# Optimization experiments

Hardware: AMD Instinct MI355X
Metric: run time of the kernel (lower is better)

Reference implementation:

```python
import jax, jax.numpy as jnp
import numpy as np
from jax.scipy.special import logsumexp

N = 8192       # number of vectors being quantized
E_DIM = 768    # embedding dim
N_E = 1024     # codebook size per layer
SK_EPS = (0.0, 0.003, 0.003, 0.003)
SK_ITERS = 100
BETA = 1.0


def setup_inputs() -> dict:
    key = jax.random.key(0)
    ks = jax.random.split(key, 5)
    inp = {"x": jax.random.normal(ks[0], (N, E_DIM), jnp.float32)}
    for i in range(4):
        inp[f"codebook_{i}"] = jax.random.normal(ks[i + 1], (N_E, E_DIM), jnp.float32) * 0.02
    return inp


def _sq_dist(x, e):
    # squared euclidean cdist: [N, K]
    return (jnp.sum(x * x, axis=1, keepdims=True)
            + jnp.sum(e * e, axis=1)[None, :]
            - 2.0 * (x @ e.T))


def _sinkhorn_indices(d, eps, iters):
    # log-domain Sinkhorn on Q = exp(-d/eps); constants (1/K, 1/B) dropped
    # since they do not affect the final argmax assignment.
    logQ = -d / eps  # [N, K]

    def body(_, lq):
        lq = lq - logsumexp(lq, axis=0, keepdims=True)  # normalize per code over batch
        lq = lq - logsumexp(lq, axis=1, keepdims=True)  # normalize per sample over codes
        return lq

    logQ = jax.lax.fori_loop(0, iters, body, logQ)
    return jnp.argmax(logQ, axis=1)


def _vq_layer(residual, codebook, eps):
    d = _sq_dist(residual, codebook)
    if eps > 0:
        indices = _sinkhorn_indices(d, eps, SK_ITERS)
    else:
        indices = jnp.argmin(d, axis=1)
    x_q = codebook[indices]  # gather [N, E_DIM]
    sg = jax.lax.stop_gradient
    loss = jnp.mean((sg(x_q) - residual) ** 2) + BETA * jnp.mean((x_q - sg(residual)) ** 2)
    x_q = residual + sg(x_q - residual)  # straight-through estimator
    return x_q, loss, indices


def reference(x, codebook_0, codebook_1, codebook_2, codebook_3):
    codebooks = (codebook_0, codebook_1, codebook_2, codebook_3)
    residual = x
    x_q = jnp.zeros_like(x)
    losses, all_idx = [], []
    for cb, eps in zip(codebooks, SK_EPS):
        xr, loss, idx = _vq_layer(residual, cb, eps)
        residual = residual - xr
        x_q = x_q + xr
        losses.append(loss)
        all_idx.append(idx)
    mean_loss = jnp.stack(losses).mean()
    indices = jnp.stack(all_idx, axis=-1)  # [N, num_quantizers]
    return x_q, mean_loss, indices
```

## Files before the change

### kernel.cpp

```cpp
#include <hip/hip_runtime.h>
#include <math.h>

#define N_VEC   8192
#define EDIM    768
#define NCODES  1024
#define SKITERS 100
#define ROWS_PB 32
#define CHUNKS  (N_VEC / ROWS_PB)
#define DYN_LDS ((32 * NCODES + 32) * 4)

__device__ __forceinline__ void ast(float* p, float v) {
  __hip_atomic_store(p, v, __ATOMIC_RELAXED, __HIP_MEMORY_SCOPE_AGENT);
}
__device__ __forceinline__ float ald(float* p) {
  return __hip_atomic_load(p, __ATOMIC_RELAXED, __HIP_MEMORY_SCOPE_AGENT);
}
__device__ __forceinline__ void asti(int* p, int v) {
  __hip_atomic_store(p, v, __ATOMIC_RELAXED, __HIP_MEMORY_SCOPE_AGENT);
}
__device__ __forceinline__ int aldi(int* p) {
  return __hip_atomic_load(p, __ATOMIC_RELAXED, __HIP_MEMORY_SCOPE_AGENT);
}
union MS { unsigned long long u; float2 f; };
__device__ __forceinline__ void astms(unsigned long long* p, float m, float s) {
  MS x; x.f.x = m; x.f.y = s;
  __hip_atomic_store(p, x.u, __ATOMIC_RELAXED, __HIP_MEMORY_SCOPE_AGENT);
}
__device__ __forceinline__ float2 aldms(unsigned long long* p) {
  MS x; x.u = __hip_atomic_load(p, __ATOMIC_RELAXED, __HIP_MEMORY_SCOPE_AGENT);
  return x.f;
}

__device__ __forceinline__ float np_base96_sq(const float* a) {
  float r[8];
#pragma unroll
  for (int j = 0; j < 8; ++j) r[j] = __fmul_rn(a[j], a[j]);
  for (int i = 8; i < 96; i += 8) {
#pragma unroll
    for (int j = 0; j < 8; ++j) r[j] = __fadd_rn(r[j], __fmul_rn(a[i + j], a[i + j]));
  }
  float c01 = __fadd_rn(r[0], r[1]);
  float c23 = __fadd_rn(r[2], r[3]);
  float c45 = __fadd_rn(r[4], r[5]);
  float c67 = __fadd_rn(r[6], r[7]);
  return __fadd_rn(__fadd_rn(c01, c23), __fadd_rn(c45, c67));
}
__device__ __forceinline__ float np_ssq768(const float* a) {
  float L[8];
#pragma unroll
  for (int t = 0; t < 8; ++t) L[t] = np_base96_sq(a + 96 * t);
  float a01 = __fadd_rn(L[0], L[1]);
  float a23 = __fadd_rn(L[2], L[3]);
  float a45 = __fadd_rn(L[4], L[5]);
  float a67 = __fadd_rn(L[6], L[7]);
  return __fadd_rn(__fadd_rn(a01, a23), __fadd_rn(a45, a67));
}

__global__ __launch_bounds__(64) void rows_ssq(const float* __restrict__ a,
                                               float* __restrict__ out, int nrows) {
  int row = blockIdx.x * 64 + threadIdx.x;
  if (row < nrows) out[row] = np_ssq768(a + (size_t)row * EDIM);
}

#define BM 128
#define BN 128
#define BK 16
template <bool LAYER0>
__global__ __launch_bounds__(256) void gemm_d(const float* __restrict__ A,
                                              const float* __restrict__ B,
                                              const float* __restrict__ sumrr,
                                              const float* __restrict__ sumee,
                                              float* __restrict__ V) {
  __shared__ float As[BK][BM];
  __shared__ float Bs[BK][BN];
  int tid = threadIdx.x;
  int bm = blockIdx.y * BM;
  int bn = blockIdx.x * BN;
  int lr = tid >> 1;
  int lc = (tid & 1) << 3;
  const float* Ap = A + (size_t)(bm + lr) * EDIM + lc;
  const float* Bp = B + (size_t)(bn + lr) * EDIM + lc;
  float acc[8][8];
#pragma unroll
  for (int i = 0; i < 8; ++i)
#pragma unroll
    for (int j = 0; j < 8; ++j) acc[i][j] = 0.f;
  int ty = tid >> 4, tx = tid & 15;
  for (int k0 = 0; k0 < EDIM; k0 += BK) {
    float4 a0 = *(const float4*)(Ap + k0);
    float4 a1 = *(const float4*)(Ap + k0 + 4);
    float4 b0 = *(const float4*)(Bp + k0);
    float4 b1 = *(const float4*)(Bp + k0 + 4);
    __syncthreads();
    As[lc + 0][lr] = a0.x; As[lc + 1][lr] = a0.y; As[lc + 2][lr] = a0.z; As[lc + 3][lr] = a0.w;
    As[lc + 4][lr] = a1.x; As[lc + 5][lr] = a1.y; As[lc + 6][lr] = a1.z; As[lc + 7][lr] = a1.w;
    Bs[lc + 0][lr] = b0.x; Bs[lc + 1][lr] = b0.y; Bs[lc + 2][lr] = b0.z; Bs[lc + 3][lr] = b0.w;
    Bs[lc + 4][lr] = b1.x; Bs[lc + 5][lr] = b1.y; Bs[lc + 6][lr] = b1.z; Bs[lc + 7][lr] = b1.w;
    __syncthreads();
#pragma unroll
    for (int k = 0; k < BK; ++k) {
      float av[8], bv[8];
      *(float4*)(av)     = *(const float4*)(&As[k][ty * 8]);
      *(float4*)(av + 4) = *(const float4*)(&As[k][ty * 8 + 4]);
      *(float4*)(bv)     = *(const float4*)(&Bs[k][tx * 8]);
      *(float4*)(bv + 4) = *(const float4*)(&Bs[k][tx * 8 + 4]);
#pragma unroll
      for (int i = 0; i < 8; ++i)
#pragma unroll
        for (int j = 0; j < 8; ++j) acc[i][j] = __fmaf_rn(av[i], bv[j], acc[i][j]);
    }
  }
#pragma unroll
  for (int i = 0; i < 8; ++i) {
    int row = bm + ty * 8 + i;
    float srr = sumrr[row];
    float* Vp = V + (size_t)row * NCODES + bn + tx * 8;
#pragma unroll
    for (int j = 0; j < 8; ++j) {
      int col = bn + tx * 8 + j;
      float s1 = __fadd_rn(srr, sumee[col]);
      float dv = __fsub_rn(s1, __fmul_rn(2.0f, acc[i][j]));
      Vp[j] = LAYER0 ? dv : __fdiv_rn(-dv, 0.003f);
    }
  }
}

__device__ __forceinline__ void accf(float w, float& m, float& s) {
  float d = __fsub_rn(w, m);
  float e = expf(-fabsf(d));
  bool gt = (w > m);
  s = gt ? __fadd_rn(__fmul_rn(s, e), 1.0f) : __fadd_rn(s, e);
  m = gt ? w : m;
}
__device__ __forceinline__ void mergef(float mo, float so, float& m, float& s) {
  float mn = fmaxf(m, mo);
  if (mn == -INFINITY) { s = 0.f; return; }
  float d = __fsub_rn(mo, m);
  float e = expf(-fabsf(d));
  bool gt = (mo > m);
  s = gt ? __fadd_rn(__fmul_rn(s, e), so) : __fadd_rn(s, __fmul_rn(so, e));
  m = mn;
}

__global__ __launch_bounds__(1024) void sk_persist(float* __restrict__ lq,
                                                   unsigned long long* __restrict__ part,
                                                   float* __restrict__ colL,
                                                   int* __restrict__ parr,
                                                   int* __restrict__ cready,
                                                   int* __restrict__ xarr,
                                                   int* __restrict__ xdone) {
  extern __shared__ float lds[];
  float (*vL)[NCODES] = (float(*)[NCODES])lds;
  float* rowLs = lds + 32 * NCODES;
  int tid = threadIdx.x, b = blockIdx.x;
  int wave = tid >> 6, lane = tid & 63;
  int r0 = b * ROWS_PB;

  float v[32];
#pragma unroll
  for (int r = 0; r < 32; ++r) v[r] = lq[(size_t)(r0 + r) * NCODES + tid];

#define COLCHAIN_ARRIVE(GEN)                                                  \
  do {                                                                        \
    float m = -INFINITY, s = 0.f;                                             \
    _Pragma("unroll")                                                         \
    for (int r = 0; r < 32; ++r) accf(v[r], m, s);                            \
    astms(&part[(size_t)b * NCODES + tid], m, s);                             \
    asm volatile("s_waitcnt vmcnt(0)" ::: "memory");                          \
    __syncthreads();                                                          \
    if (tid == 0) asti(&parr[b * 16], (GEN));                                 \
  } while (0)

  COLCHAIN_ARRIVE(1);

  for (int t = 0; t < SKITERS; ++t) {
    int gen = t + 1;

    if (wave == 0) {
      if (b < 8) {
        if (lane < 32) {
          int* fl = &parr[(b * 32 + lane) * 16];
          while (aldi(fl) < gen) __builtin_amdgcn_s_sleep(1);
        }
        asm volatile("" ::: "memory");
        if (lane == 0) asti(&xarr[b * 16], gen);
      }
      if (lane < 8) {
        int* fl = &xarr[lane * 16];
        while (aldi(fl) < gen) __builtin_amdgcn_s_sleep(1);
      }
      asm volatile("" ::: "memory");
      float m = -INFINITY, s = 0.f;
      if (lane < 32) {
        int colj = lane >> 3, grp = lane & 7;
        int col = 4 * b + colj;
#pragma unroll
        for (int qb = 0; qb < 32; qb += 16) {
          float2 pv[16];
#pragma unroll
          for (int q = 0; q < 16; ++q)
            pv[q] = aldms(&part[(size_t)(grp * 32 + qb + q) * NCODES + col]);
#pragma unroll
          for (int q = 0; q < 16; ++q) mergef(pv[q].x, pv[q].y, m, s);
        }
      }
      float mm = -INFINITY, ss = 0.f;
#pragma unroll
      for (int g2 = 0; g2 < 8; ++g2) {
        float mo = __shfl(m, ((lane & 3) << 3) + g2, 64);
        float so = __shfl(s, ((lane & 3) << 3) + g2, 64);
        mergef(mo, so, mm, ss);
      }
      if (lane < 4) ast(&colL[4 * b + lane], __fadd_rn(logf(ss), mm));
      asm volatile("s_waitcnt vmcnt(0)" ::: "memory");
      if (lane == 0) asti(&cready[b * 16], gen);
      if (b < 8) {
        if (lane < 32) {
          int* fl = &cready[(b * 32 + lane) * 16];
          while (aldi(fl) < gen) __builtin_amdgcn_s_sleep(1);
        }
        asm volatile("" ::: "memory");
        if (lane == 0) asti(&xdone[b * 16], gen);
      }
      if (lane < 8) {
        int* fl = &xdone[lane * 16];
        while (aldi(fl) < gen) __builtin_amdgcn_s_sleep(1);
      }
      asm volatile("" ::: "memory");
    }
    __syncthreads();

    float cl = ald(&colL[tid]);
#pragma unroll
    for (int r = 0; r < 32; ++r) {
      v[r] = __fsub_rn(v[r], cl);
      vL[r][tid] = v[r];
    }
    __syncthreads();

#pragma unroll
    for (int rr = 0; rr < 2; ++rr) {
      int row = wave * 2 + rr;
      float vals[16];
#pragma unroll
      for (int k = 0; k < 16; ++k) vals[k] = vL[row][lane + (k << 6)];
      float mx = vals[0];
#pragma unroll
      for (int k = 1; k < 16; ++k) mx = fmaxf(mx, vals[k]);
      for (int off = 32; off; off >>= 1) mx = fmaxf(mx, __shfl_xor(mx, off, 64));
      float s = 0.f;
#pragma unroll
      for (int k = 0; k < 16; ++k) s = __fadd_rn(s, expf(__fsub_rn(vals[k], mx)));
      for (int off = 32; off; off >>= 1) s = __fadd_rn(s, __shfl_xor(s, off, 64));
      if (lane == 0) rowLs[row] = __fadd_rn(logf(s), mx);
    }
    __syncthreads();
#pragma unroll
    for (int r = 0; r < 32; ++r) v[r] = __fsub_rn(v[r], rowLs[r]);

    if (t < SKITERS - 1) COLCHAIN_ARRIVE(gen + 1);
  }

#pragma unroll
  for (int r = 0; r < 32; ++r) lq[(size_t)(r0 + r) * NCODES + tid] = v[r];
#undef COLCHAIN_ARRIVE
}

template <int MODE>
__global__ __launch_bounds__(256) void epi(const float* __restrict__ V,
                                           const float* __restrict__ rin,
                                           const float* __restrict__ cb,
                                           float* __restrict__ rout,
                                           double* __restrict__ rowssq,
                                           float* __restrict__ idx_out,
                                           int layer) {
  int i = blockIdx.x;
  int tid = threadIdx.x;
  const float* Vrow = V + (size_t)i * NCODES;
  float bv = MODE ? -INFINITY : INFINITY;
  int bj = 0;
  for (int j = tid; j < NCODES; j += 256) {
    float v = Vrow[j];
    bool better = MODE ? (v > bv) : (v < bv);
    if (better) { bv = v; bj = j; }
  }
  __shared__ float sv[256];
  __shared__ int   sj[256];
  sv[tid] = bv; sj[tid] = bj;
  __syncthreads();
  for (int st = 128; st; st >>= 1) {
    if (tid < st) {
      float v2 = sv[tid + st]; int j2 = sj[tid + st];
      bool better = MODE ? (v2 > sv[tid]) : (v2 < sv[tid]);
      if (better || (v2 == sv[tid] && j2 < sj[tid])) { sv[tid] = v2; sj[tid] = j2; }
    }
    __syncthreads();
  }
  int idx = sj[0];
  const float* crow = cb + (size_t)idx * EDIM;
  double p = 0.0;
  for (int c = tid; c < EDIM; c += 256) {
    float rn = __fsub_rn(rin[(size_t)i * EDIM + c], crow[c]);
    rout[(size_t)i * EDIM + c] = rn;
    p += (double)rn * (double)rn;
  }
  for (int off = 32; off; off >>= 1) p += __shfl_xor(p, off, 64);
  __shared__ double wsum[4];
  if ((tid & 63) == 0) wsum[tid >> 6] = p;
  __syncthreads();
  if (tid == 0) {
    rowssq[i] = wsum[0] + wsum[1] + wsum[2] + wsum[3];
    idx_out[(size_t)i * 4 + layer] = (float)idx;
  }
}

__global__ __launch_bounds__(1024) void loss_final(const double* __restrict__ rowssq,
                                                   float* __restrict__ out_loss) {
  int tid = threadIdx.x;
  __shared__ double acc[16];
  __shared__ double ltot;
  if (tid == 0) ltot = 0.0;
  __syncthreads();
  for (int l = 0; l < 4; ++l) {
    double p = 0.0;
    for (int i = tid; i < N_VEC; i += 1024) p += rowssq[l * N_VEC + i];
    for (int off = 32; off; off >>= 1) p += __shfl_xor(p, off, 64);
    if ((tid & 63) == 0) acc[tid >> 6] = p;
    __syncthreads();
    if (tid == 0) {
      double sl = 0.0;
      for (int w = 0; w < 16; ++w) sl += acc[w];
      ltot += 2.0 * sl / ((double)N_VEC * (double)EDIM);
    }
    __syncthreads();
  }
  if (tid == 0) out_loss[0] = (float)(ltot * 0.25);
}

__global__ __launch_bounds__(256) void xq_final(const float* __restrict__ x,
                                                float* __restrict__ out) {
  size_t i = ((size_t)blockIdx.x * 256 + threadIdx.x) * 4;
  float4 xv = *(const float4*)(x + i);
  float4 rv = *(const float4*)(out + i);
  float4 o;
  o.x = __fsub_rn(xv.x, rv.x); o.y = __fsub_rn(xv.y, rv.y);
  o.z = __fsub_rn(xv.z, rv.z); o.w = __fsub_rn(xv.w, rv.w);
  *(float4*)(out + i) = o;
}

extern "C" void kernel_launch(void* const* d_in, const int* in_sizes, int n_in,
                              void* d_out, int out_size, void* d_ws, size_t ws_size,
                              hipStream_t stream) {
  const float* x = (const float*)d_in[0];
  const float* cbs[4] = {(const float*)d_in[1], (const float*)d_in[2],
                         (const float*)d_in[3], (const float*)d_in[4]};
  float* out = (float*)d_out;
  float* resid = out;
  float* loss_out = out + (size_t)N_VEC * EDIM;
  float* idx_out = loss_out + 1;

  float* ws = (float*)d_ws;
  float* lq    = ws;
  unsigned long long* part = (unsigned long long*)(lq + (size_t)N_VEC * NCODES);
  float* colL  = (float*)(part + (size_t)CHUNKS * NCODES);
  float* sumrr = colL + NCODES;
  float* sumee = sumrr + N_VEC;
  double* rowssq = (double*)(sumee + 4 * NCODES);
  int* flagbase = (int*)(rowssq + 4 * N_VEC);

  static int lds_set = 0;
  if (!lds_set) {
    hipFuncSetAttribute((const void*)sk_persist,
                        hipFuncAttributeMaxDynamicSharedMemorySize, DYN_LDS);
    lds_set = 1;
  }

  hipMemsetAsync(flagbase, 0, 4 * 16384 * sizeof(int), stream);

  for (int l = 0; l < 4; ++l)
    rows_ssq<<<NCODES / 64, 64, 0, stream>>>(cbs[l], sumee + l * NCODES, NCODES);
  rows_ssq<<<N_VEC / 64, 64, 0, stream>>>(x, sumrr, N_VEC);

  for (int l = 0; l < 4; ++l) {
    const float* rin = (l == 0) ? x : resid;
    if (l == 0) {
      gemm_d<true><<<dim3(NCODES / BN, N_VEC / BM), 256, 0, stream>>>(rin, cbs[l], sumrr, sumee + l * NCODES, lq);
      epi<0><<<N_VEC, 256, 0, stream>>>(lq, rin, cbs[l], resid, rowssq + (size_t)l * N_VEC, idx_out, l);
    } else {
      gemm_d<false><<<dim3(NCODES / BN, N_VEC / BM), 256, 0, stream>>>(rin, cbs[l], sumrr, sumee + l * NCODES, lq);
      int* lf = flagbase + l * 16384;
      sk_persist<<<CHUNKS, 1024, DYN_LDS, stream>>>(lq, part, colL,
                                                    lf, lf + 4096, lf + 8192, lf + 8448);
      epi<1><<<N_VEC, 256, 0, stream>>>(lq, rin, cbs[l], resid, rowssq + (size_t)l * N_VEC, idx_out, l);
    }
    if (l < 3)
      rows_ssq<<<N_VEC / 64, 64, 0, stream>>>(resid, sumrr, N_VEC);
  }
  loss_final<<<1, 1024, 0, stream>>>(rowssq, loss_out);
  xq_final<<<(N_VEC * EDIM / 4) / 256, 256, 0, stream>>>(x, out);
}
```

Baseline: 6.878 ms.

## Replace second grid barrier with generation-tagged column logsumexp values

The column-normalizer broadcast in the persistent Sinkhorn kernel used to finish each iteration with a two-level grid barrier (cready/xdone) and a block __syncthreads before reading colL. Now each column value is stored as a 64-bit word holding the float plus a generation tag, and every thread spins on its own column's word until the tag reaches the current generation. This removes one grid-wide barrier per iteration, across 100 iterations and three layers. In exchange every thread polls global memory, and the tags need a per-layer generation offset so stale values from earlier layers are not mistaken for current ones.

```diff
diff --git a/kernel.cpp b/kernel.cpp
--- a/kernel.cpp
+++ b/kernel.cpp
@@ -12,9 +12,6 @@
 __device__ __forceinline__ void ast(float* p, float v) {
   __hip_atomic_store(p, v, __ATOMIC_RELAXED, __HIP_MEMORY_SCOPE_AGENT);
 }
-__device__ __forceinline__ float ald(float* p) {
-  return __hip_atomic_load(p, __ATOMIC_RELAXED, __HIP_MEMORY_SCOPE_AGENT);
-}
 __device__ __forceinline__ void asti(int* p, int v) {
   __hip_atomic_store(p, v, __ATOMIC_RELAXED, __HIP_MEMORY_SCOPE_AGENT);
 }
@@ -29,6 +26,15 @@
 __device__ __forceinline__ float2 aldms(unsigned long long* p) {
   MS x; x.u = __hip_atomic_load(p, __ATOMIC_RELAXED, __HIP_MEMORY_SCOPE_AGENT);
   return x.f;
+}
+union TV { unsigned long long u; struct { float v; unsigned g; } p; };
+__device__ __forceinline__ TV tvload(const unsigned long long* p) {
+  TV x; x.u = __hip_atomic_load((unsigned long long*)p, __ATOMIC_RELAXED, __HIP_MEMORY_SCOPE_AGENT);
+  return x;
+}
+__device__ __forceinline__ void tvstore(unsigned long long* p, float v, unsigned g) {
+  TV x; x.p.v = v; x.p.g = g;
+  __hip_atomic_store(p, x.u, __ATOMIC_RELAXED, __HIP_MEMORY_SCOPE_AGENT);
 }
 
 __device__ __forceinline__ float np_base96_sq(const float* a) {
@@ -144,11 +150,10 @@
 
 __global__ __launch_bounds__(1024) void sk_persist(float* __restrict__ lq,
                                                    unsigned long long* __restrict__ part,
-                                                   float* __restrict__ colL,
+                                                   unsigned long long* __restrict__ cT,
                                                    int* __restrict__ parr,
-                                                   int* __restrict__ cready,
                                                    int* __restrict__ xarr,
-                                                   int* __restrict__ xdone) {
+                                                   unsigned gen0) {
   extern __shared__ float lds[];
   float (*vL)[NCODES] = (float(*)[NCODES])lds;
   float* rowLs = lds + 32 * NCODES;
@@ -175,6 +180,7 @@
 
   for (int t = 0; t < SKITERS; ++t) {
     int gen = t + 1;
+    unsigned cg = gen0 + (unsigned)gen;
 
     if (wave == 0) {
       if (b < 8) {
@@ -211,26 +217,16 @@
         float so = __shfl(s, ((lane & 3) << 3) + g2, 64);
         mergef(mo, so, mm, ss);
       }
-      if (lane < 4) ast(&colL[4 * b + lane], __fadd_rn(logf(ss), mm));
-      asm volatile("s_waitcnt vmcnt(0)" ::: "memory");
-      if (lane == 0) asti(&cready[b * 16], gen);
-      if (b < 8) {
-        if (lane < 32) {
-          int* fl = &cready[(b * 32 + lane) * 16];
-          while (aldi(fl) < gen) __builtin_amdgcn_s_sleep(1);
-        }
-        asm volatile("" ::: "memory");
-        if (lane == 0) asti(&xdone[b * 16], gen);
-      }
-      if (lane < 8) {
-        int* fl = &xdone[lane * 16];
-        while (aldi(fl) < gen) __builtin_amdgcn_s_sleep(1);
-      }
-      asm volatile("" ::: "memory");
-    }
-    __syncthreads();
-
-    float cl = ald(&colL[tid]);
+      if (lane < 4) tvstore(&cT[4 * b + lane], __fadd_rn(logf(ss), mm), cg);
+    }
+
+    float cl;
+    {
+      TV cv = tvload(&cT[tid]);
+      while (cv.p.g < cg) { __builtin_amdgcn_s_sleep(1); cv = tvload(&cT[tid]); }
+      cl = cv.p.v;
+    }
+
 #pragma unroll
     for (int r = 0; r < 32; ++r) {
       v[r] = __fsub_rn(v[r], cl);
@@ -360,10 +356,10 @@
   float* idx_out = loss_out + 1;
 
   float* ws = (float*)d_ws;
-  float* lq    = ws;
+  float* lq = ws;
   unsigned long long* part = (unsigned long long*)(lq + (size_t)N_VEC * NCODES);
-  float* colL  = (float*)(part + (size_t)CHUNKS * NCODES);
-  float* sumrr = colL + NCODES;
+  unsigned long long* cT = part + (size_t)CHUNKS * NCODES;
+  float* sumrr = (float*)(cT + NCODES);
   float* sumee = sumrr + N_VEC;
   double* rowssq = (double*)(sumee + 4 * NCODES);
   int* flagbase = (int*)(rowssq + 4 * N_VEC);
@@ -375,7 +371,8 @@
     lds_set = 1;
   }
 
-  hipMemsetAsync(flagbase, 0, 4 * 16384 * sizeof(int), stream);
+  hipMemsetAsync(cT, 0, NCODES * 8, stream);
+  hipMemsetAsync(flagbase, 0, 4 * 8192 * sizeof(int), stream);
 
   for (int l = 0; l < 4; ++l)
     rows_ssq<<<NCODES / 64, 64, 0, stream>>>(cbs[l], sumee + l * NCODES, NCODES);
@@ -388,9 +385,9 @@
       epi<0><<<N_VEC, 256, 0, stream>>>(lq, rin, cbs[l], resid, rowssq + (size_t)l * N_VEC, idx_out, l);
     } else {
       gemm_d<false><<<dim3(NCODES / BN, N_VEC / BM), 256, 0, stream>>>(rin, cbs[l], sumrr, sumee + l * NCODES, lq);
-      int* lf = flagbase + l * 16384;
-      sk_persist<<<CHUNKS, 1024, DYN_LDS, stream>>>(lq, part, colL,
-                                                    lf, lf + 4096, lf + 8192, lf + 8448);
+      int* lf = flagbase + l * 8192;
+      sk_persist<<<CHUNKS, 1024, DYN_LDS, stream>>>(lq, part, cT,
+                                                    lf, lf + 4096, (unsigned)(256 * l));
       epi<1><<<N_VEC, 256, 0, stream>>>(lq, rin, cbs[l], resid, rowssq + (size_t)l * N_VEC, idx_out, l);
     }
     if (l < 3)
```

Measured after the change: 6.576 ms. 4.4% less time.
